# Performance work log

Hardware: AMD Instinct MI355X
Metric: run time of the kernel (lower is better)

Reference implementation:

```python
import jax, jax.numpy as jnp
import numpy as np
from jax import lax

N, H, W = 16, 112, 112
CIN, COUT, K = 256, 256, 3
STRIDE, PAD = 1, 1


def setup_inputs() -> dict:
    key = jax.random.key(0)
    kx, kw = jax.random.split(key)
    # int8-valued activations and weights, stored as int32 for portable integer conv
    x = jax.random.randint(kx, (N, H, W, CIN), -128, 128, dtype=jnp.int32)
    # weight layout matches the torch module: (out_channels, kH, kW, in_channels) == OHWI
    weight = jax.random.randint(kw, (COUT, K, K, CIN), -128, 128, dtype=jnp.int32)
    return {"x": x, "weight": weight}


def reference(x, weight):
    y = lax.conv_general_dilated(
        x,
        weight,
        window_strides=(STRIDE, STRIDE),
        padding=[(PAD, PAD), (PAD, PAD)],
        dimension_numbers=("NHWC", "OHWI", "NHWC"),
        preferred_element_type=jnp.int32,
    )
    return y  # (N, H, W, COUT) int32
```

## Files before the change

kernel.cpp:

```cpp
#include <hip/hip_runtime.h>
#include <stdint.h>

#define NN   16
#define HH   112
#define WW   112
#define CIN  256
#define COUT 256
#define HP   114
#define WP   114
#define M_TOTAL (NN * HH * WW)
#define XP_BYTES ((size_t)NN * HP * WP * CIN)
#define WPK_BYTES ((size_t)9 * COUT * CIN)

typedef int v4i __attribute__((ext_vector_type(4)));

__device__ __forceinline__ void load_lds16(const void* g, void* l) {
  __builtin_amdgcn_global_load_lds(
      (const __attribute__((address_space(1))) void*)g,
      (__attribute__((address_space(3))) void*)l, 16, 0, 0);
}

__device__ __forceinline__ int pack4(int a, int b, int c, int d) {
  return (a & 255) | ((b & 255) << 8) | ((c & 255) << 16) | (d << 24);
}

__global__ void pack_x_kernel(const int* __restrict__ x, char* __restrict__ xp) {
  int t = blockIdx.x * 256 + threadIdx.x;
  int c4 = t & 63;
  int p = t >> 6;
  int w = p % WW;
  int t2 = p / WW;
  int h = t2 % HH;
  int n = t2 / HH;
  int4 v = *(const int4*)(x + (size_t)t * 4);
  int ov = pack4(v.x, v.y, v.z, v.w);
  size_t dst = (((size_t)n * HP + (h + 1)) * WP + (w + 1)) * CIN + (size_t)c4 * 4;
  *(int*)(xp + dst) = ov;
}

__global__ void zero_border_kernel(char* __restrict__ xp) {
  int t = blockIdx.x * 256 + threadIdx.x;
  int g = t & 15;
  int pix = t >> 4;
  int n = pix / 452;
  int b = pix % 452;
  int h, w;
  if (b < 114) { h = 0; w = b; }
  else if (b < 228) { h = 113; w = b - 114; }
  else { int r = b - 228; h = 1 + (r >> 1); w = (r & 1) ? 113 : 0; }
  size_t dst = (((size_t)n * HP + h) * WP + w) * CIN + (size_t)g * 16;
  *(int4*)(xp + dst) = make_int4(0, 0, 0, 0);
}

__global__ void pack_w_kernel(const int* __restrict__ wgt, char* __restrict__ wp) {
  int t = blockIdx.x * 256 + threadIdx.x;
  int c4 = t & 63;
  int r = t >> 6;
  int tap = r % 9;
  int cout = r / 9;
  int4 v = *(const int4*)(wgt + (size_t)t * 4);
  int ov = pack4(v.x, v.y, v.z, v.w);
  size_t dst = ((size_t)tap * COUT + cout) * CIN + (size_t)c4 * 4;
  *(int*)(wp + dst) = ov;
}

__global__ __launch_bounds__(256, 2) void conv_mfma_kernel(const char* __restrict__ xp,
                                                           const char* __restrict__ wp,
                                                           int* __restrict__ out) {
  __shared__ __align__(16) char As[2 * 128 * 64];
  __shared__ __align__(16) char Bs[2 * 256 * 64];
  const int tid = threadIdx.x;
  const int lane = tid & 63;
  const int wave = tid >> 6;
  const int mtile = blockIdx.x;

  const char* gptr[6];
  char* lptr[6];
  int  isA[6];
#pragma unroll
  for (int j = 0; j < 6; j++) {
    int c = wave * 6 + j;
    if (c < 8) {
      int row = c * 16 + (lane >> 2);
      int colg = (lane & 3) ^ ((row >> 1) & 3);
      int m = mtile * 128 + row;
      int w = m % WW;
      int t2 = m / WW;
      int h = t2 % HH;
      int n = t2 / HH;
      gptr[j] = xp + (((size_t)n * HP + h) * WP + w) * CIN + (size_t)colg * 16;
      lptr[j] = As + c * 1024;
      isA[j] = 1;
    } else {
      int cb = c - 8;
      int row = cb * 16 + (lane >> 2);
      int colg = (lane & 3) ^ ((row >> 1) & 3);
      gptr[j] = wp + (size_t)row * CIN + (size_t)colg * 16;
      lptr[j] = Bs + cb * 1024;
      isA[j] = 0;
    }
  }

  const int wm = wave & 1;
  const int wn = wave >> 1;
  int aoff[4], boff[8];
#pragma unroll
  for (int i = 0; i < 4; i++) {
    int ra = wm * 64 + i * 16 + (lane & 15);
    aoff[i] = ra * 64 + (((lane >> 4) ^ ((ra >> 1) & 3)) * 16);
  }
#pragma unroll
  for (int j = 0; j < 8; j++) {
    int rb = wn * 128 + j * 16 + (lane & 15);
    boff[j] = rb * 64 + (((lane >> 4) ^ ((rb >> 1) & 3)) * 16);
  }

  v4i acc[4][8];
#pragma unroll
  for (int i = 0; i < 4; i++)
#pragma unroll
    for (int j = 0; j < 8; j++) acc[i][j] = (v4i){0, 0, 0, 0};

  auto stage = [&](int ks, int b) {
    int tap = ks >> 2;
    int kb = ks & 3;
    int ky = tap / 3;
    int kx = tap - ky * 3;
    int offA = (ky * WP + kx) * CIN + kb * 64;
    int offB = tap * (COUT * CIN) + kb * 64;
#pragma unroll
    for (int j = 0; j < 6; j++)
      load_lds16(gptr[j] + (isA[j] ? offA : offB),
                 lptr[j] + (isA[j] ? b * 8192 : b * 16384));
  };

  stage(0, 0);

#pragma unroll 1
  for (int ks = 0; ks < 36; ks++) {
    const int cur = ks & 1;
    __syncthreads();
    if (ks + 1 < 36) stage(ks + 1, cur ^ 1);
    const char* Ab = As + cur * 8192;
    const char* Bb = Bs + cur * 16384;
    v4i af[4], bf[8];
#pragma unroll
    for (int i = 0; i < 4; i++) af[i] = *(const v4i*)(Ab + aoff[i]);
#pragma unroll
    for (int j = 0; j < 8; j++) bf[j] = *(const v4i*)(Bb + boff[j]);
#pragma unroll
    for (int i = 0; i < 4; i++)
#pragma unroll
      for (int j = 0; j < 8; j++)
        acc[i][j] = __builtin_amdgcn_mfma_i32_16x16x64_i8(af[i], bf[j], acc[i][j], 0, 0, 0);
  }

#pragma unroll
  for (int i = 0; i < 4; i++) {
    const int mg = mtile * 128 + wm * 64 + i * 16 + ((lane >> 4) * 4);
#pragma unroll
    for (int r = 0; r < 4; r++) {
      int* orow = out + (size_t)(mg + r) * COUT + wn * 128 + (lane & 15);
#pragma unroll
      for (int j = 0; j < 8; j++) orow[j * 16] = acc[i][j][r];
    }
  }
}

__global__ void conv_naive_kernel(const int* __restrict__ x, const int* __restrict__ wgt,
                                  int* __restrict__ out, int total) {
  int idx = blockIdx.x * 256 + threadIdx.x;
  if (idx >= total) return;
  int co = idx & 255;
  int p = idx >> 8;
  int w = p % WW;
  int t2 = p / WW;
  int h = t2 % HH;
  int n = t2 / HH;
  int acc = 0;
  for (int ky = 0; ky < 3; ky++) {
    int ih = h + ky - 1;
    if (ih < 0 || ih >= HH) continue;
    for (int kx = 0; kx < 3; kx++) {
      int iw = w + kx - 1;
      if (iw < 0 || iw >= WW) continue;
      const int* xs = x + (((size_t)n * HH + ih) * WW + iw) * CIN;
      const int* ws = wgt + ((size_t)co * 9 + ky * 3 + kx) * CIN;
      for (int ci = 0; ci < CIN; ci++) acc += xs[ci] * ws[ci];
    }
  }
  out[idx] = acc;
}

extern "C" void kernel_launch(void* const* d_in, const int* in_sizes, int n_in,
                              void* d_out, int out_size, void* d_ws, size_t ws_size,
                              hipStream_t stream) {
  const int* x = (const int*)d_in[0];
  const int* wgt = (const int*)d_in[1];
  int* out = (int*)d_out;
  const size_t need = XP_BYTES + WPK_BYTES;
  if (ws_size >= need) {
    char* xp = (char*)d_ws;
    char* wp = xp + XP_BYTES;
    pack_x_kernel<<<(M_TOTAL * 64) / 256, 256, 0, stream>>>(x, xp);
    zero_border_kernel<<<(7232 * 16) / 256, 256, 0, stream>>>(xp);
    pack_w_kernel<<<(2304 * 64) / 256, 256, 0, stream>>>(wgt, wp);
    conv_mfma_kernel<<<M_TOTAL / 128, 256, 0, stream>>>(xp, wp, out);
  } else {
    conv_naive_kernel<<<(out_size + 255) / 256, 256, 0, stream>>>(x, wgt, out, out_size);
  }
}
```

Baseline: 462.6 us.

## Triple-buffer conv LDS pipeline, vectorize x packing, merge weight and border kernels

The MFMA conv kernel moves from a double to a triple-buffered LDS pipeline that prefetches two k-steps ahead. Each step's global-to-LDS loads are split into halves interleaved with two MFMA phases, using explicit vmcnt/lgkmcnt waits, barriers and setprio, so memory latency overlaps with compute. The x packing kernel now has each thread write 16 bytes instead of 4, and the weight pack and border-zero kernels are merged into one launch. The cost is more LDS per block (about 72KB for two blocks per CU) and hand-tuned wait counts that are fragile if the number of outstanding loads changes.

```diff
diff --git a/kernel.cpp b/kernel.cpp
--- a/kernel.cpp
+++ b/kernel.cpp
@@ -26,49 +26,56 @@
 
 __global__ void pack_x_kernel(const int* __restrict__ x, char* __restrict__ xp) {
   int t = blockIdx.x * 256 + threadIdx.x;
-  int c4 = t & 63;
-  int p = t >> 6;
+  int g = t & 15;
+  int p = t >> 4;
   int w = p % WW;
   int t2 = p / WW;
   int h = t2 % HH;
   int n = t2 / HH;
-  int4 v = *(const int4*)(x + (size_t)t * 4);
-  int ov = pack4(v.x, v.y, v.z, v.w);
-  size_t dst = (((size_t)n * HP + (h + 1)) * WP + (w + 1)) * CIN + (size_t)c4 * 4;
-  *(int*)(xp + dst) = ov;
-}
-
-__global__ void zero_border_kernel(char* __restrict__ xp) {
-  int t = blockIdx.x * 256 + threadIdx.x;
-  int g = t & 15;
-  int pix = t >> 4;
-  int n = pix / 452;
-  int b = pix % 452;
-  int h, w;
-  if (b < 114) { h = 0; w = b; }
-  else if (b < 228) { h = 113; w = b - 114; }
-  else { int r = b - 228; h = 1 + (r >> 1); w = (r & 1) ? 113 : 0; }
-  size_t dst = (((size_t)n * HP + h) * WP + w) * CIN + (size_t)g * 16;
-  *(int4*)(xp + dst) = make_int4(0, 0, 0, 0);
-}
-
-__global__ void pack_w_kernel(const int* __restrict__ wgt, char* __restrict__ wp) {
-  int t = blockIdx.x * 256 + threadIdx.x;
-  int c4 = t & 63;
-  int r = t >> 6;
-  int tap = r % 9;
-  int cout = r / 9;
-  int4 v = *(const int4*)(wgt + (size_t)t * 4);
-  int ov = pack4(v.x, v.y, v.z, v.w);
-  size_t dst = ((size_t)tap * COUT + cout) * CIN + (size_t)c4 * 4;
-  *(int*)(wp + dst) = ov;
+  const int4* src = (const int4*)(x + (size_t)t * 16);
+  int4 a = src[0], b = src[1], c = src[2], d = src[3];
+  int4 ov;
+  ov.x = pack4(a.x, a.y, a.z, a.w);
+  ov.y = pack4(b.x, b.y, b.z, b.w);
+  ov.z = pack4(c.x, c.y, c.z, c.w);
+  ov.w = pack4(d.x, d.y, d.z, d.w);
+  size_t dst = (((size_t)n * HP + (h + 1)) * WP + (w + 1)) * CIN + (size_t)g * 16;
+  *(int4*)(xp + dst) = ov;
+}
+
+__global__ void pack_w_border_kernel(const int* __restrict__ wgt, char* __restrict__ xp,
+                                     char* __restrict__ wp) {
+  int bid = blockIdx.x;
+  if (bid < 576) {
+    int t = bid * 256 + threadIdx.x;
+    int c4 = t & 63;
+    int r = t >> 6;
+    int tap = r % 9;
+    int cout = r / 9;
+    int4 v = *(const int4*)(wgt + (size_t)t * 4);
+    int ov = pack4(v.x, v.y, v.z, v.w);
+    size_t dst = ((size_t)tap * COUT + cout) * CIN + (size_t)c4 * 4;
+    *(int*)(wp + dst) = ov;
+  } else {
+    int t = (bid - 576) * 256 + threadIdx.x;
+    int g = t & 15;
+    int pix = t >> 4;
+    int n = pix / 452;
+    int b = pix % 452;
+    int h, w;
+    if (b < 114) { h = 0; w = b; }
+    else if (b < 228) { h = 113; w = b - 114; }
+    else { int r = b - 228; h = 1 + (r >> 1); w = (r & 1) ? 113 : 0; }
+    size_t dst = (((size_t)n * HP + h) * WP + w) * CIN + (size_t)g * 16;
+    *(int4*)(xp + dst) = make_int4(0, 0, 0, 0);
+  }
 }
 
 __global__ __launch_bounds__(256, 2) void conv_mfma_kernel(const char* __restrict__ xp,
                                                            const char* __restrict__ wp,
                                                            int* __restrict__ out) {
-  __shared__ __align__(16) char As[2 * 128 * 64];
-  __shared__ __align__(16) char Bs[2 * 256 * 64];
+  __shared__ __align__(16) char As[3 * 128 * 64];
+  __shared__ __align__(16) char Bs[3 * 256 * 64];
   const int tid = threadIdx.x;
   const int lane = tid & 63;
   const int wave = tid >> 6;
@@ -121,7 +128,7 @@
 #pragma unroll
     for (int j = 0; j < 8; j++) acc[i][j] = (v4i){0, 0, 0, 0};
 
-  auto stage = [&](int ks, int b) {
+  auto stage_half = [&](int ks, int b, int half) {
     int tap = ks >> 2;
     int kb = ks & 3;
     int ky = tap / 3;
@@ -129,30 +136,59 @@
     int offA = (ky * WP + kx) * CIN + kb * 64;
     int offB = tap * (COUT * CIN) + kb * 64;
 #pragma unroll
-    for (int j = 0; j < 6; j++)
+    for (int j = half * 3; j < half * 3 + 3; j++)
       load_lds16(gptr[j] + (isA[j] ? offA : offB),
                  lptr[j] + (isA[j] ? b * 8192 : b * 16384));
   };
 
-  stage(0, 0);
-
+  stage_half(0, 0, 0); stage_half(0, 0, 1);
+  stage_half(1, 1, 0); stage_half(1, 1, 1);
+  asm volatile("s_waitcnt vmcnt(6)" ::: "memory");
+  __builtin_amdgcn_s_barrier();
+
+  int bc = 0;
+  int bs = 2;
 #pragma unroll 1
   for (int ks = 0; ks < 36; ks++) {
-    const int cur = ks & 1;
-    __syncthreads();
-    if (ks + 1 < 36) stage(ks + 1, cur ^ 1);
-    const char* Ab = As + cur * 8192;
-    const char* Bb = Bs + cur * 16384;
+    const char* Ab = As + bc * 8192;
+    const char* Bb = Bs + bc * 16384;
     v4i af[4], bf[8];
+
 #pragma unroll
     for (int i = 0; i < 4; i++) af[i] = *(const v4i*)(Ab + aoff[i]);
 #pragma unroll
-    for (int j = 0; j < 8; j++) bf[j] = *(const v4i*)(Bb + boff[j]);
+    for (int j = 0; j < 4; j++) bf[j] = *(const v4i*)(Bb + boff[j]);
+    if (ks < 34) stage_half(ks + 2, bs, 0);
+    __builtin_amdgcn_s_barrier();
+    asm volatile("s_waitcnt lgkmcnt(0)" ::: "memory");
+    __builtin_amdgcn_s_setprio(1);
 #pragma unroll
     for (int i = 0; i < 4; i++)
 #pragma unroll
-      for (int j = 0; j < 8; j++)
+      for (int j = 0; j < 4; j++)
         acc[i][j] = __builtin_amdgcn_mfma_i32_16x16x64_i8(af[i], bf[j], acc[i][j], 0, 0, 0);
+    __builtin_amdgcn_s_setprio(0);
+    __builtin_amdgcn_s_barrier();
+
+#pragma unroll
+    for (int j = 4; j < 8; j++) bf[j] = *(const v4i*)(Bb + boff[j]);
+    if (ks < 34) stage_half(ks + 2, bs, 1);
+    __builtin_amdgcn_s_barrier();
+    asm volatile("s_waitcnt lgkmcnt(0)" ::: "memory");
+    __builtin_amdgcn_s_setprio(1);
+#pragma unroll
+    for (int i = 0; i < 4; i++)
+#pragma unroll
+      for (int j = 4; j < 8; j++)
+        acc[i][j] = __builtin_amdgcn_mfma_i32_16x16x64_i8(af[i], bf[j], acc[i][j], 0, 0, 0);
+    __builtin_amdgcn_s_setprio(0);
+
+    if (ks < 34)       asm volatile("s_waitcnt vmcnt(6)" ::: "memory");
+    else if (ks == 34) asm volatile("s_waitcnt vmcnt(0)" ::: "memory");
+    __builtin_amdgcn_s_barrier();
+
+    bc = (bc == 2) ? 0 : bc + 1;
+    bs = (bs == 2) ? 0 : bs + 1;
   }
 
 #pragma unroll
@@ -202,9 +238,8 @@
   if (ws_size >= need) {
     char* xp = (char*)d_ws;
     char* wp = xp + XP_BYTES;
-    pack_x_kernel<<<(M_TOTAL * 64) / 256, 256, 0, stream>>>(x, xp);
-    zero_border_kernel<<<(7232 * 16) / 256, 256, 0, stream>>>(xp);
-    pack_w_kernel<<<(2304 * 64) / 256, 256, 0, stream>>>(wgt, wp);
+    pack_x_kernel<<<(M_TOTAL * 16) / 256, 256, 0, stream>>>(x, xp);
+    pack_w_border_kernel<<<576 + 452, 256, 0, stream>>>(wgt, xp, wp);
     conv_mfma_kernel<<<M_TOTAL / 128, 256, 0, stream>>>(xp, wp, out);
   } else {
     conv_naive_kernel<<<(out_size + 255) / 256, 256, 0, stream>>>(x, wgt, out, out_size);
```

After: 465.5 us. No clear change (+0.6%).
